# Kernel tuning notes

Hardware: AMD Instinct MI355X
Metric: run time of the kernel (lower is better)

The kernel has to match this reference:

```python
import jax, jax.numpy as jnp
import numpy as np

HALF = 6.0
MAXC = 63.0
M_EMA = 0.999

def _pooled_ema(feature, pre, fea):
    # feature: [b,c,64,64]; pre: [b,21,2] float coords; fea: [21,c] EMA state
    b, c, H, W = feature.shape
    x = pre[..., 0]
    y = pre[..., 1]
    # torch: clamp then .int() (truncation == floor for non-negative values)
    down = jnp.maximum(y - HALF, 0.0).astype(jnp.int32)   # [b,21]
    left = jnp.maximum(x - HALF, 0.0).astype(jnp.int32)
    upper = jnp.minimum(y + HALF, MAXC).astype(jnp.int32)
    right = jnp.minimum(x + HALF, MAXC).astype(jnp.int32)
    # divisor uses inclusive window size (s1*s2), even though the torch slice
    # feature[:, left:right, down:upper] is exclusive at right/upper (faithful quirk)
    s = ((upper - down + 1) * (right - left + 1)).astype(feature.dtype)  # [b,21]
    # integral image (padded) -> rectangle sum over [left,right) x [down,upper)
    P = jnp.pad(jnp.cumsum(jnp.cumsum(feature, axis=2), axis=3),
                ((0, 0), (0, 0), (1, 0), (1, 0)))  # [b,c,H+1,W+1]
    bi = jnp.arange(b)[:, None]  # [b,1] broadcasts with [b,21] indices
    rect = (P[bi, :, right, upper] - P[bi, :, left, upper]
            - P[bi, :, right, down] + P[bi, :, left, down])  # [b,21,c]
    f4 = rect / s[..., None]          # per-landmark average pool [b,21,c]
    fea_c = f4.mean(axis=0)           # average over batch -> [21,c]
    return M_EMA * fea_c + (1.0 - M_EMA) * fea


def setup_inputs() -> dict:
    key = jax.random.key(0)
    k1, k2, k3, k4 = jax.random.split(key, 4)
    b, c, H, W, L = 64, 256, 64, 64, 21
    f1 = jax.random.uniform(k1, (b, c, H, W), dtype=jnp.float32)
    f2 = jax.random.uniform(k2, (b, c, H, W), dtype=jnp.float32)
    pre1 = jax.random.uniform(k3, (b, L, 2), dtype=jnp.float32) * 63.0
    pre2 = jax.random.uniform(k4, (b, L, 2), dtype=jnp.float32) * 63.0
    fea1 = jnp.zeros((L, c), dtype=jnp.float32)
    fea2 = jnp.zeros((L, c), dtype=jnp.float32)
    return {"f1": f1, "f2": f2, "pre1": pre1, "pre2": pre2,
            "fea1": fea1, "fea2": fea2}


def reference(f1, f2, pre1, pre2, fea1, fea2):
    fea_c1 = _pooled_ema(f1, pre1, fea1)               # [21,c]
    log_p = jax.nn.log_softmax(fea_c1, axis=-1)
    fea_c2 = _pooled_ema(f2, pre2, fea2)               # [21,c]
    q = fea_c2 / fea_c2.sum(axis=-1, keepdims=True)
    # KLDivLoss(reduction='none'): q * (log q - log_p), zero where q == 0
    kl = jnp.where(q > 0, q * (jnp.log(jnp.where(q > 0, q, 1.0)) - log_p), 0.0)
    return kl.sum(axis=-1).mean()
```

## Files before the change

### kernel.cpp

```cpp
#include <hip/hip_runtime.h>

#define NL 21
#define NC 256
#define NB 64
#define PSTRIDE 72
#define PPB 16

__global__ __launch_bounds__(256, 8) void pool_kernel(
    const float* __restrict__ f1, const float* __restrict__ f2,
    const float* __restrict__ pre1, const float* __restrict__ pre2,
    float* __restrict__ part1, float* __restrict__ part2) {
    const int p0   = blockIdx.x * PPB;
    const int feat = p0 >> 14;
    const int b    = (p0 >> 8) & 63;
    const int c0   = p0 & 255;
    const float* __restrict__ base = (feat ? f2 : f1) + (size_t)(b * NC + c0) * 4096;
    const float* __restrict__ pre  = feat ? pre2 : pre1;
    float* __restrict__ outp       = (feat ? part2 : part1) + (size_t)b * NL * NC;

    __shared__ float buf[64 * PSTRIDE];
    __shared__ int s_left[NL], s_right[NL], s_down[NL], s_upper[NL];
    __shared__ float s_invs[NL];

    const int t    = threadIdx.x;
    const int wv   = t >> 6;
    const int lane = t & 63;
    const int rr   = lane >> 4;
    const int cc   = lane & 15;

    if (t < NL) {
        const float x = pre[(b * NL + t) * 2 + 0];
        const float y = pre[(b * NL + t) * 2 + 1];
        const int down  = (int)fmaxf(y - 6.0f, 0.0f);
        const int left  = (int)fmaxf(x - 6.0f, 0.0f);
        const int upper = (int)fminf(y + 6.0f, 63.0f);
        const int right = (int)fminf(x + 6.0f, 63.0f);
        s_left[t] = left; s_right[t] = right; s_down[t] = down; s_upper[t] = upper;
        s_invs[t] = 1.0f / (float)((upper - down + 1) * (right - left + 1));
    }

    float4 v0, v1, v2, v3;
    {
        const float4* __restrict__ src = (const float4*)base;
        v0 = src[t]; v1 = src[t + 256]; v2 = src[t + 512]; v3 = src[t + 768];
        *(float4*)&buf[((t      ) >> 4) * PSTRIDE + ((t      ) & 15) * 4] = v0;
        *(float4*)&buf[((t + 256) >> 4) * PSTRIDE + ((t + 256) & 15) * 4] = v1;
        *(float4*)&buf[((t + 512) >> 4) * PSTRIDE + ((t + 512) & 15) * 4] = v2;
        *(float4*)&buf[((t + 768) >> 4) * PSTRIDE + ((t + 768) & 15) * 4] = v3;
    }
    __syncthreads();

    for (int i = 0; i < PPB; ++i) {
        if (i + 1 < PPB) {
            const float4* __restrict__ src = (const float4*)(base + (size_t)(i + 1) * 4096);
            v0 = src[t]; v1 = src[t + 256]; v2 = src[t + 512]; v3 = src[t + 768];
        }
        for (int l = wv; l < NL; l += 4) {
            const int d = s_down[l], u = s_upper[l];
            const int L = s_left[l], R = s_right[l];
            const int col = d + cc;
            float s = 0.0f;
            if (col < u) {
                const float* __restrict__ rowp = &buf[col];
#pragma unroll
                for (int p = 0; p < 3; ++p) {
                    const int row = L + p * 4 + rr;
                    if (row < R) s += rowp[row * PSTRIDE];
                }
            }
#pragma unroll
            for (int o = 32; o > 0; o >>= 1) s += __shfl_xor(s, o, 64);
            if (lane == 0) outp[l * NC + (c0 + i)] = s * s_invs[l];
        }
        __syncthreads();
        if (i + 1 < PPB) {
            *(float4*)&buf[((t      ) >> 4) * PSTRIDE + ((t      ) & 15) * 4] = v0;
            *(float4*)&buf[((t + 256) >> 4) * PSTRIDE + ((t + 256) & 15) * 4] = v1;
            *(float4*)&buf[((t + 512) >> 4) * PSTRIDE + ((t + 512) & 15) * 4] = v2;
            *(float4*)&buf[((t + 768) >> 4) * PSTRIDE + ((t + 768) & 15) * 4] = v3;
        }
        __syncthreads();
    }
}

__global__ __launch_bounds__(256) void reduce_kernel(
    const float* __restrict__ part1, const float* __restrict__ part2,
    const float* __restrict__ fea1, const float* __restrict__ fea2,
    float* __restrict__ sc ) {
    const int f = blockIdx.x / NL;
    const int l = blockIdx.x - f * NL;
    const int c = threadIdx.x;
    const float* __restrict__ part = f ? part2 : part1;
    const float* __restrict__ fea  = f ? fea2 : fea1;
    float s = 0.0f;
    for (int b = 0; b < NB; ++b) s += part[((size_t)b * NL + l) * NC + c];
    sc[(f * NL + l) * NC + c] = 0.999f * (s * (1.0f / 64.0f)) + 0.001f * fea[l * NC + c];
}

__global__ __launch_bounds__(256) void finish_kernel(const float* __restrict__ sc,
                                                     float* __restrict__ out) {
    const int t = threadIdx.x;
    const int wave = t >> 6, lane = t & 63;
    __shared__ float rowkl[NL];

    for (int l = wave; l < NL; l += 4) {
        const float* __restrict__ r1 = &sc[l * NC];
        const float* __restrict__ r2 = &sc[(NL + l) * NC];
        float x1[4], x2[4];
#pragma unroll
        for (int j = 0; j < 4; ++j) { x1[j] = r1[lane + 64 * j]; x2[j] = r2[lane + 64 * j]; }

        float m  = fmaxf(fmaxf(x1[0], x1[1]), fmaxf(x1[2], x1[3]));
        float s2 = x2[0] + x2[1] + x2[2] + x2[3];
#pragma unroll
        for (int o = 32; o > 0; o >>= 1) {
            m  = fmaxf(m, __shfl_xor(m, o, 64));
            s2 += __shfl_xor(s2, o, 64);
        }
        float es = 0.0f;
#pragma unroll
        for (int j = 0; j < 4; ++j) es += __expf(x1[j] - m);
#pragma unroll
        for (int o = 32; o > 0; o >>= 1) es += __shfl_xor(es, o, 64);
        const float logZ = m + logf(es);
        const float inv_s2 = 1.0f / s2;

        float kl = 0.0f;
#pragma unroll
        for (int j = 0; j < 4; ++j) {
            const float q = x2[j] * inv_s2;
            if (q > 0.0f) kl += q * (logf(q) - (x1[j] - logZ));
        }
#pragma unroll
        for (int o = 32; o > 0; o >>= 1) kl += __shfl_xor(kl, o, 64);
        if (lane == 0) rowkl[l] = kl;
    }
    __syncthreads();
    if (t == 0) {
        float tot = 0.0f;
        for (int l = 0; l < NL; ++l) tot += rowkl[l];
        out[0] = tot / 21.0f;
    }
}

extern "C" void kernel_launch(void* const* d_in, const int* in_sizes, int n_in,
                              void* d_out, int out_size, void* d_ws, size_t ws_size,
                              hipStream_t stream) {
    const float* f1   = (const float*)d_in[0];
    const float* f2   = (const float*)d_in[1];
    const float* pre1 = (const float*)d_in[2];
    const float* pre2 = (const float*)d_in[3];
    const float* fea1 = (const float*)d_in[4];
    const float* fea2 = (const float*)d_in[5];
    float* out = (float*)d_out;

    float* part1 = (float*)d_ws;
    float* part2 = part1 + (size_t)NB * NL * NC;
    float* sc    = part2 + (size_t)NB * NL * NC;

    pool_kernel<<<dim3(2 * NB * NC / PPB), 256, 0, stream>>>(f1, f2, pre1, pre2, part1, part2);
    reduce_kernel<<<dim3(2 * NL), 256, 0, stream>>>(part1, part2, fea1, fea2, sc);
    finish_kernel<<<1, 256, 0, stream>>>(sc, out);
}
```

Measured before the change: 542.4 us.

## Gather landmark windows directly from global memory instead of staging planes in LDS

The pool kernel no longer copies each full 64x64 channel plane into shared memory. Each 16-thread group now precomputes clamped offsets and masks for up to two landmarks and gathers only the window elements straight from global memory, reducing with 16-lane shuffles. This removes the full-plane reads, the LDS staging and the block barriers. In exchange it relies on scattered, poorly coalesced global loads with little reuse, and overlapping windows hit the caches repeatedly.

```diff
diff --git a/kernel.cpp b/kernel.cpp
--- a/kernel.cpp
+++ b/kernel.cpp
@@ -3,10 +3,9 @@
 #define NL 21
 #define NC 256
 #define NB 64
-#define PSTRIDE 72
 #define PPB 16
 
-__global__ __launch_bounds__(256, 8) void pool_kernel(
+__global__ __launch_bounds__(256) void pool_kernel(
     const float* __restrict__ f1, const float* __restrict__ f2,
     const float* __restrict__ pre1, const float* __restrict__ pre2,
     float* __restrict__ part1, float* __restrict__ part2) {
@@ -16,70 +15,73 @@
     const int c0   = p0 & 255;
     const float* __restrict__ base = (feat ? f2 : f1) + (size_t)(b * NC + c0) * 4096;
     const float* __restrict__ pre  = feat ? pre2 : pre1;
-    float* __restrict__ outp       = (feat ? part2 : part1) + (size_t)b * NL * NC;
-
-    __shared__ float buf[64 * PSTRIDE];
-    __shared__ int s_left[NL], s_right[NL], s_down[NL], s_upper[NL];
-    __shared__ float s_invs[NL];
+    float* __restrict__ outp       = (feat ? part2 : part1) + (size_t)b * NL * NC + c0;
 
     const int t    = threadIdx.x;
-    const int wv   = t >> 6;
-    const int lane = t & 63;
-    const int rr   = lane >> 4;
-    const int cc   = lane & 15;
+    const int slot = t >> 4;
+    const int li   = t & 15;
+    const int ro   = li >> 2;
+    const int co   = li & 3;
 
-    if (t < NL) {
-        const float x = pre[(b * NL + t) * 2 + 0];
-        const float y = pre[(b * NL + t) * 2 + 1];
+    int   boff[2][9];
+    float msk[2][9];
+    float inv[2];
+    int   lrow[2];
+    bool  valid[2];
+
+#pragma unroll
+    for (int pp = 0; pp < 2; ++pp) {
+        const int l = slot + 16 * pp;
+        valid[pp] = (l < NL);
+        const int lc = valid[pp] ? l : NL - 1;
+        lrow[pp] = lc;
+        const float x = pre[(b * NL + lc) * 2 + 0];
+        const float y = pre[(b * NL + lc) * 2 + 1];
         const int down  = (int)fmaxf(y - 6.0f, 0.0f);
         const int left  = (int)fmaxf(x - 6.0f, 0.0f);
         const int upper = (int)fminf(y + 6.0f, 63.0f);
         const int right = (int)fminf(x + 6.0f, 63.0f);
-        s_left[t] = left; s_right[t] = right; s_down[t] = down; s_upper[t] = upper;
-        s_invs[t] = 1.0f / (float)((upper - down + 1) * (right - left + 1));
+        const int RL = right - left;
+        const int UD = upper - down;
+        inv[pp] = 1.0f / (float)((UD + 1) * (RL + 1));
+        int rowc[3], colc[3];
+        float rm[3], cm[3];
+#pragma unroll
+        for (int p = 0; p < 3; ++p) {
+            const int a = ro + 4 * p;
+            rm[p]   = (valid[pp] && a < RL) ? 1.0f : 0.0f;
+            rowc[p] = left + (a < RL ? a : RL - 1);
+            const int c = co + 4 * p;
+            cm[p]   = (c < UD) ? 1.0f : 0.0f;
+            colc[p] = down + (c < UD ? c : UD - 1);
+        }
+#pragma unroll
+        for (int p = 0; p < 3; ++p)
+#pragma unroll
+            for (int q = 0; q < 3; ++q) {
+                boff[pp][p * 3 + q] = ((rowc[p] << 6) + colc[q]) << 2;
+                msk[pp][p * 3 + q]  = rm[p] * cm[q];
+            }
     }
 
-    float4 v0, v1, v2, v3;
-    {
-        const float4* __restrict__ src = (const float4*)base;
-        v0 = src[t]; v1 = src[t + 256]; v2 = src[t + 512]; v3 = src[t + 768];
-        *(float4*)&buf[((t      ) >> 4) * PSTRIDE + ((t      ) & 15) * 4] = v0;
-        *(float4*)&buf[((t + 256) >> 4) * PSTRIDE + ((t + 256) & 15) * 4] = v1;
-        *(float4*)&buf[((t + 512) >> 4) * PSTRIDE + ((t + 512) & 15) * 4] = v2;
-        *(float4*)&buf[((t + 768) >> 4) * PSTRIDE + ((t + 768) & 15) * 4] = v3;
-    }
-    __syncthreads();
-
     for (int i = 0; i < PPB; ++i) {
-        if (i + 1 < PPB) {
-            const float4* __restrict__ src = (const float4*)(base + (size_t)(i + 1) * 4096);
-            v0 = src[t]; v1 = src[t + 256]; v2 = src[t + 512]; v3 = src[t + 768];
+        const char* __restrict__ pc = (const char*)base + (size_t)i * 16384;
+        float s0 = 0.0f, s1 = 0.0f;
+#pragma unroll
+        for (int k = 0; k < 9; ++k)
+            s0 = fmaf(msk[0][k], *(const float*)(pc + boff[0][k]), s0);
+#pragma unroll
+        for (int k = 0; k < 9; ++k)
+            s1 = fmaf(msk[1][k], *(const float*)(pc + boff[1][k]), s1);
+#pragma unroll
+        for (int o = 8; o > 0; o >>= 1) {
+            s0 += __shfl_xor(s0, o, 16);
+            s1 += __shfl_xor(s1, o, 16);
         }
-        for (int l = wv; l < NL; l += 4) {
-            const int d = s_down[l], u = s_upper[l];
-            const int L = s_left[l], R = s_right[l];
-            const int col = d + cc;
-            float s = 0.0f;
-            if (col < u) {
-                const float* __restrict__ rowp = &buf[col];
-#pragma unroll
-                for (int p = 0; p < 3; ++p) {
-                    const int row = L + p * 4 + rr;
-                    if (row < R) s += rowp[row * PSTRIDE];
-                }
-            }
-#pragma unroll
-            for (int o = 32; o > 0; o >>= 1) s += __shfl_xor(s, o, 64);
-            if (lane == 0) outp[l * NC + (c0 + i)] = s * s_invs[l];
+        if (li == 0) {
+            outp[lrow[0] * NC + i] = s0 * inv[0];
+            if (valid[1]) outp[lrow[1] * NC + i] = s1 * inv[1];
         }
-        __syncthreads();
-        if (i + 1 < PPB) {
-            *(float4*)&buf[((t      ) >> 4) * PSTRIDE + ((t      ) & 15) * 4] = v0;
-            *(float4*)&buf[((t + 256) >> 4) * PSTRIDE + ((t + 256) & 15) * 4] = v1;
-            *(float4*)&buf[((t + 512) >> 4) * PSTRIDE + ((t + 512) & 15) * 4] = v2;
-            *(float4*)&buf[((t + 768) >> 4) * PSTRIDE + ((t + 768) & 15) * 4] = v3;
-        }
-        __syncthreads();
     }
 }
 
```

Measured after the change: 597.2 us. +10.1%, slower.
